# Optimization experiments

Hardware: AMD Instinct MI355X
Metric: run time of the kernel (lower is better)

Reference implementation:

```python
import jax, jax.numpy as jnp
import numpy as np

EPS = 1e-12  # F.normalize default eps


def _wn_weight(v, g):
    # PyTorch weight_norm over dims (in, kernel) per output channel
    norm = jnp.sqrt(jnp.sum(v * v, axis=1, keepdims=True))
    return g[:, None] * v / norm


def _l2_normalize(x, axis=-1):
    n = jnp.sqrt(jnp.sum(x * x, axis=axis, keepdims=True))
    return x / jnp.maximum(n, EPS)


def setup_inputs() -> dict:
    key = jax.random.key(0)
    ks = jax.random.split(key, 8)
    B, D_IN, T = 16, 1024, 2048
    K, D_CB = 4096, 256
    s = 0.02
    return {
        "z": jax.random.normal(ks[0], (B, D_IN, T), dtype=jnp.float32),
        "in_v": jax.random.normal(ks[1], (D_CB, D_IN), dtype=jnp.float32) * s,
        "in_g": jax.random.uniform(ks[2], (D_CB,), dtype=jnp.float32, minval=0.5, maxval=1.5),
        "in_b": jax.random.normal(ks[3], (D_CB,), dtype=jnp.float32) * s,
        "out_v": jax.random.normal(ks[4], (D_IN, D_CB), dtype=jnp.float32) * s,
        "out_g": jax.random.uniform(ks[5], (D_IN,), dtype=jnp.float32, minval=0.5, maxval=1.5),
        "out_b": jax.random.normal(ks[6], (D_IN,), dtype=jnp.float32) * s,
        "codebook": jax.random.normal(ks[7], (K, D_CB), dtype=jnp.float32),
    }


def reference(z, in_v, in_g, in_b, out_v, out_g, out_b, codebook):
    B, _, T = z.shape
    # in_proj: weight-normalized 1x1 conv == per-frame matmul
    W_in = _wn_weight(in_v, in_g)            # (D_cb, D_in)
    z_i = jnp.einsum("oc,bct->bot", W_in, z) + in_b[None, :, None]  # (B, D_cb, T)

    # decode_latents: factorized, L2-normalized nearest-neighbor lookup
    enc = z_i.transpose(0, 2, 1).reshape(-1, z_i.shape[1])  # (B*T, D_cb)
    enc_n = _l2_normalize(enc)
    cb_n = _l2_normalize(codebook)
    dist = (
        jnp.sum(enc_n * enc_n, axis=1, keepdims=True)
        - 2.0 * enc_n @ cb_n.T
        + jnp.sum(cb_n * cb_n, axis=1)[None, :]
    )  # (B*T, K)
    indices = jnp.argmax(-dist, axis=1).reshape(B, T)       # (B, T)
    z_q = codebook[indices].transpose(0, 2, 1)              # (B, D_cb, T)

    # straight-through estimator
    z_q = z_i + jax.lax.stop_gradient(z_q - z_i)

    # out_proj
    W_out = _wn_weight(out_v, out_g)         # (D_in, D_cb)
    z_o = jnp.einsum("oc,bct->bot", W_out, z_q) + out_b[None, :, None]  # (B, D_in, T)
    return (z_i, z_q, z_o, indices)
```

## Files before the change

kernel.cpp:

```cpp
#include <hip/hip_runtime.h>
#include <hip/hip_bf16.h>

#define BATCH 16
#define D_IN  1024
#define T_LEN 2048
#define K_CB  4096
#define D_CB  256

#define ZI_OFF 0
#define ZQ_OFF (BATCH * D_CB * T_LEN)
#define ZO_OFF (ZQ_OFF + BATCH * D_CB * T_LEN)
#define IDX_OFF (ZO_OFF + BATCH * D_IN * T_LEN)

typedef _Float16 half8 __attribute__((ext_vector_type(8)));
typedef _Float16 h4_t  __attribute__((ext_vector_type(4)));
typedef float floatx4 __attribute__((ext_vector_type(4)));

__device__ __forceinline__ float block_sum256(float v) {
    __shared__ float sred[4];
    #pragma unroll
    for (int off = 32; off > 0; off >>= 1) v += __shfl_down(v, off, 64);
    if ((threadIdx.x & 63) == 0) sred[threadIdx.x >> 6] = v;
    __syncthreads();
    float r = sred[0] + sred[1] + sred[2] + sred[3];
    __syncthreads();
    return r;
}

__global__ __launch_bounds__(256) void wn_rows(const float* __restrict__ v,
                                               const float* __restrict__ g,
                                               float* __restrict__ W, int N) {
    int row = blockIdx.x;
    const float* src = v + (size_t)row * N;
    float ss = 0.f;
    for (int c = threadIdx.x; c < N; c += 256) { float x = src[c]; ss += x * x; }
    ss = block_sum256(ss);
    float scale = g[row] * __frsqrt_rn(ss);
    for (int c = threadIdx.x; c < N; c += 256) W[(size_t)row * N + c] = src[c] * scale;
}

__global__ __launch_bounds__(256) void cb_prep(const float* __restrict__ cb,
                                               _Float16* __restrict__ c1,
                                               _Float16* __restrict__ c2) {
    int row = blockIdx.x;
    int c = threadIdx.x;
    float x = cb[(size_t)row * D_CB + c];
    float ss = block_sum256(x * x);
    float scale = 1.0f / fmaxf(sqrtf(ss), 1e-12f);
    float v = x * scale;
    _Float16 h1 = (_Float16)v;
    _Float16 h2 = (_Float16)(v - (float)h1);
    c1[(size_t)row * D_CB + c] = h1;
    c2[(size_t)row * D_CB + c] = h2;
}

template <int KDIM, int M>
__global__ __launch_bounds__(256, 2) void proj_mfma(const float* __restrict__ W,
                                                    const float* __restrict__ bias,
                                                    const float* __restrict__ Z,
                                                    float* __restrict__ Out) {
    __shared__ _Float16 A_s[2][128][40];
    __shared__ _Float16 B_s[2][128][40];

    const int tid  = threadIdx.x;
    const int wv   = tid >> 6;
    const int lane = tid & 63;
    const int lo4  = lane & 15, quad = lane >> 4;
    const int wm   = wv & 1,  wn  = wv >> 1;

    const int f0 = blockIdx.x * 128;
    const int b  = f0 >> 11;
    const int t0 = f0 & (T_LEN - 1);
    const int o0 = blockIdx.y * 128;
    const float* __restrict__ Zb = Z + (size_t)b * KDIM * T_LEN;

    const int a_g  = tid >> 5;
    const int a_tl = tid & 31;

    float  pa[4][4];
    float4 pb[4];

    floatx4 acc[4][4];
    #pragma unroll
    for (int i = 0; i < 4; i++)
        #pragma unroll
        for (int j = 0; j < 4; j++) acc[i][j] = (floatx4){0.f, 0.f, 0.f, 0.f};

    #pragma unroll
    for (int p = 0; p < 4; p++)
        #pragma unroll
        for (int j = 0; j < 4; j++)
            pa[p][j] = Zb[(size_t)(a_g * 4 + j) * T_LEN + t0 + p * 32 + a_tl];
    #pragma unroll
    for (int p = 0; p < 4; p++) {
        int idx = tid + p * 256;
        pb[p] = *(const float4*)&W[(size_t)(o0 + (idx >> 3)) * KDIM + (idx & 7) * 4];
    }

    for (int kk = 0; kk < KDIM; kk += 32) {
        #pragma unroll
        for (int p = 0; p < 4; p++) {
            int f = p * 32 + a_tl;
            h4_t h1, h2;
            #pragma unroll
            for (int j = 0; j < 4; j++) {
                float v = pa[p][j];
                _Float16 x = (_Float16)v;
                h1[j] = x;
                h2[j] = (_Float16)(v - (float)x);
            }
            *(h4_t*)&A_s[0][f][a_g * 4] = h1;
            *(h4_t*)&A_s[1][f][a_g * 4] = h2;
        }
        #pragma unroll
        for (int p = 0; p < 4; p++) {
            int idx = tid + p * 256;
            int o = idx >> 3, k4 = (idx & 7) * 4;
            h4_t h1, h2;
            #pragma unroll
            for (int j = 0; j < 4; j++) {
                float v = ((const float*)&pb[p])[j];
                _Float16 x = (_Float16)v;
                h1[j] = x;
                h2[j] = (_Float16)(v - (float)x);
            }
            *(h4_t*)&B_s[0][o][k4] = h1;
            *(h4_t*)&B_s[1][o][k4] = h2;
        }
        __syncthreads();

        if (kk + 32 < KDIM) {
            #pragma unroll
            for (int p = 0; p < 4; p++)
                #pragma unroll
                for (int j = 0; j < 4; j++)
                    pa[p][j] = Zb[(size_t)(kk + 32 + a_g * 4 + j) * T_LEN + t0 + p * 32 + a_tl];
            #pragma unroll
            for (int p = 0; p < 4; p++) {
                int idx = tid + p * 256;
                pb[p] = *(const float4*)&W[(size_t)(o0 + (idx >> 3)) * KDIM + kk + 32 + (idx & 7) * 4];
            }
        }

        half8 a1[4], a2[4], b1[4], b2[4];
        #pragma unroll
        for (int mi = 0; mi < 4; mi++) {
            a1[mi] = *(const half8*)&A_s[0][wm * 64 + mi * 16 + lo4][quad * 8];
            a2[mi] = *(const half8*)&A_s[1][wm * 64 + mi * 16 + lo4][quad * 8];
        }
        #pragma unroll
        for (int ni = 0; ni < 4; ni++) {
            b1[ni] = *(const half8*)&B_s[0][wn * 64 + ni * 16 + lo4][quad * 8];
            b2[ni] = *(const half8*)&B_s[1][wn * 64 + ni * 16 + lo4][quad * 8];
        }
        #pragma unroll
        for (int mi = 0; mi < 4; mi++)
            #pragma unroll
            for (int ni = 0; ni < 4; ni++) {
                acc[mi][ni] = __builtin_amdgcn_mfma_f32_16x16x32_f16(a1[mi], b1[ni], acc[mi][ni], 0, 0, 0);
                acc[mi][ni] = __builtin_amdgcn_mfma_f32_16x16x32_f16(a1[mi], b2[ni], acc[mi][ni], 0, 0, 0);
                acc[mi][ni] = __builtin_amdgcn_mfma_f32_16x16x32_f16(a2[mi], b1[ni], acc[mi][ni], 0, 0, 0);
            }
        __syncthreads();
    }

    #pragma unroll
    for (int ni = 0; ni < 4; ni++) {
        int o = o0 + wn * 64 + ni * 16 + lo4;
        float bv = bias[o];
        #pragma unroll
        for (int mi = 0; mi < 4; mi++) {
            int t = t0 + wm * 64 + mi * 16 + quad * 4;
            floatx4 r = acc[mi][ni];
            float4 st = make_float4(r[0] + bv, r[1] + bv, r[2] + bv, r[3] + bv);
            *(float4*)&Out[((size_t)b * M + o) * T_LEN + t] = st;
        }
    }
}

__global__ __launch_bounds__(256) void vq_mfma(const float* __restrict__ z_i,
                                               const _Float16* __restrict__ cbn1,
                                               const _Float16* __restrict__ cbn2,
                                               const float* __restrict__ cb,
                                               float* __restrict__ z_q,
                                               float* __restrict__ idx_out) {
    __shared__ _Float16 e_s[2][32][264];
    __shared__ _Float16 cb_s[2][128][72];
    __shared__ float red_v[4][32];
    __shared__ int   red_i[4][32];
    __shared__ int   idx_s[32];

    const int tid  = threadIdx.x;
    const int wv   = tid >> 6;
    const int lane = tid & 63;
    const int lo4  = lane & 15, quad = lane >> 4;
    const int f0 = blockIdx.x * 32;
    const int b  = f0 >> 11;
    const int t0 = f0 & (T_LEN - 1);

    for (int i = tid; i < 32 * 256; i += 256) {
        int k = i >> 5, t = i & 31;
        float v = z_i[((size_t)(b * D_CB + k)) * T_LEN + t0 + t];
        _Float16 h1 = (_Float16)v;
        _Float16 h2 = (_Float16)(v - (float)h1);
        e_s[0][t][k] = h1;
        e_s[1][t][k] = h2;
    }

    float best_v[2][4];
    int   best_i[2][4];
    #pragma unroll
    for (int m = 0; m < 2; m++)
        #pragma unroll
        for (int r = 0; r < 4; r++) { best_v[m][r] = -3.4e38f; best_i[m][r] = 0; }

    __syncthreads();

    for (int n = 0; n < 32; n++) {
        const int cwg = n * 128;
        floatx4 acc[2][2];
        #pragma unroll
        for (int m = 0; m < 2; m++)
            #pragma unroll
            for (int t = 0; t < 2; t++) acc[m][t] = (floatx4){0.f, 0.f, 0.f, 0.f};

        half8 pf[8];
        #pragma unroll
        for (int s = 0; s < 8; s++) {
            int c2 = tid + s * 256;
            const _Float16* src = (s < 4) ? cbn1 : cbn2;
            int rem = c2 & 1023, cw = rem >> 3, ko = (rem & 7) * 8;
            pf[s] = *(const half8*)(src + (size_t)(cwg + cw) * D_CB + ko);
        }

        for (int kc = 0; kc < 4; kc++) {
            #pragma unroll
            for (int s = 0; s < 8; s++) {
                int c2 = tid + s * 256;
                int sp = (s < 4) ? 0 : 1;
                int rem = c2 & 1023, cw = rem >> 3, ko = (rem & 7) * 8;
                *(half8*)&cb_s[sp][cw][ko] = pf[s];
            }
            __syncthreads();
            if (kc < 3) {
                #pragma unroll
                for (int s = 0; s < 8; s++) {
                    int c2 = tid + s * 256;
                    const _Float16* src = (s < 4) ? cbn1 : cbn2;
                    int rem = c2 & 1023, cw = rem >> 3, ko = (rem & 7) * 8;
                    pf[s] = *(const half8*)(src + (size_t)(cwg + cw) * D_CB + (kc + 1) * 64 + ko);
                }
            }
            #pragma unroll
            for (int ks = 0; ks < 2; ks++) {
                const int kb = kc * 64 + ks * 32 + quad * 8;
                const int kl = ks * 32 + quad * 8;
                half8 a1[2], a2[2], b1[2], b2[2];
                #pragma unroll
                for (int m = 0; m < 2; m++) {
                    a1[m] = *(const half8*)&e_s[0][m * 16 + lo4][kb];
                    a2[m] = *(const half8*)&e_s[1][m * 16 + lo4][kb];
                }
                #pragma unroll
                for (int t = 0; t < 2; t++) {
                    b1[t] = *(const half8*)&cb_s[0][wv * 32 + t * 16 + lo4][kl];
                    b2[t] = *(const half8*)&cb_s[1][wv * 32 + t * 16 + lo4][kl];
                }
                #pragma unroll
                for (int m = 0; m < 2; m++)
                    #pragma unroll
                    for (int t = 0; t < 2; t++) {
                        acc[m][t] = __builtin_amdgcn_mfma_f32_16x16x32_f16(a1[m], b1[t], acc[m][t], 0, 0, 0);
                        acc[m][t] = __builtin_amdgcn_mfma_f32_16x16x32_f16(a1[m], b2[t], acc[m][t], 0, 0, 0);
                        acc[m][t] = __builtin_amdgcn_mfma_f32_16x16x32_f16(a2[m], b1[t], acc[m][t], 0, 0, 0);
                    }
            }
            __syncthreads();
        }

        #pragma unroll
        for (int m = 0; m < 2; m++)
            #pragma unroll
            for (int t = 0; t < 2; t++) {
                int cwi = cwg + wv * 32 + t * 16 + lo4;
                #pragma unroll
                for (int r = 0; r < 4; r++) {
                    float v = acc[m][t][r];
                    if (v > best_v[m][r] || (v == best_v[m][r] && cwi < best_i[m][r])) {
                        best_v[m][r] = v; best_i[m][r] = cwi;
                    }
                }
            }
    }

    #pragma unroll
    for (int m = 0; m < 2; m++)
        #pragma unroll
        for (int r = 0; r < 4; r++) {
            float bv = best_v[m][r]; int bi = best_i[m][r];
            #pragma unroll
            for (int off = 8; off > 0; off >>= 1) {
                float ov = __shfl_down(bv, off, 16);
                int   oi = __shfl_down(bi, off, 16);
                if (ov > bv || (ov == bv && oi < bi)) { bv = ov; bi = oi; }
            }
            if (lo4 == 0) {
                red_v[wv][m * 16 + quad * 4 + r] = bv;
                red_i[wv][m * 16 + quad * 4 + r] = bi;
            }
        }
    __syncthreads();
    if (tid < 32) {
        float bv = red_v[0][tid]; int bi = red_i[0][tid];
        #pragma unroll
        for (int w = 1; w < 4; w++) {
            float ov = red_v[w][tid]; int oi = red_i[w][tid];
            if (ov > bv || (ov == bv && oi < bi)) { bv = ov; bi = oi; }
        }
        idx_s[tid] = bi;
        idx_out[f0 + tid] = (float)bi;
    }
    __syncthreads();

    for (int i = tid; i < 32 * 256; i += 256) {
        int k = i >> 5, t = i & 31;
        z_q[((size_t)(b * D_CB + k)) * T_LEN + t0 + t] = cb[(size_t)idx_s[t] * D_CB + k];
    }
}

extern "C" void kernel_launch(void* const* d_in, const int* in_sizes, int n_in,
                              void* d_out, int out_size, void* d_ws, size_t ws_size,
                              hipStream_t stream) {
    const float* z     = (const float*)d_in[0];
    const float* in_v  = (const float*)d_in[1];
    const float* in_g  = (const float*)d_in[2];
    const float* in_b  = (const float*)d_in[3];
    const float* out_v = (const float*)d_in[4];
    const float* out_g = (const float*)d_in[5];
    const float* out_b = (const float*)d_in[6];
    const float* cb    = (const float*)d_in[7];

    float* ws    = (float*)d_ws;
    float* W_in  = ws;
    float* W_out = ws + 262144;
    _Float16* cbn1 = (_Float16*)(ws + 524288);
    _Float16* cbn2 = (_Float16*)(ws + 1048576);

    float* out  = (float*)d_out;
    float* z_i  = out + ZI_OFF;
    float* z_q  = out + ZQ_OFF;
    float* z_o  = out + ZO_OFF;
    float* idxf = out + IDX_OFF;

    wn_rows<<<D_CB, 256, 0, stream>>>(in_v, in_g, W_in, D_IN);
    wn_rows<<<D_IN, 256, 0, stream>>>(out_v, out_g, W_out, D_CB);
    cb_prep<<<K_CB, 256, 0, stream>>>(cb, cbn1, cbn2);

    proj_mfma<D_IN, D_CB><<<dim3((BATCH * T_LEN) / 128, D_CB / 128), 256, 0, stream>>>(W_in, in_b, z, z_i);

    vq_mfma<<<(BATCH * T_LEN) / 32, 256, 0, stream>>>(z_i, cbn1, cbn2, cb, z_q, idxf);

    proj_mfma<D_CB, D_IN><<<dim3((BATCH * T_LEN) / 128, D_IN / 128), 256, 0, stream>>>(W_out, out_b, z_q, z_o);
}
```

Baseline: 691.5 us.

## Pre-swizzle codebook into MFMA fragment layout and stream it directly to registers

The codebook prep kernel now writes the hi/lo fp16 split of the normalized codebook in a tiled layout matching the MFMA B-operand fragment order, interleaving hi and lo parts. The VQ kernel drops the shared-memory codebook staging and its barriers. It keeps the full A fragments (encodings) in registers and has each wave stream its own slice of the codebook from global/L2 with a one-tile register prefetch. Splitting the accumulators into two chains adds MFMA independence, and launch bounds request two blocks per CU. The cost is much higher register pressure and no shared reuse of codebook data across the four waves, so global/L2 traffic goes up.

```diff
diff --git a/kernel.cpp b/kernel.cpp
--- a/kernel.cpp
+++ b/kernel.cpp
@@ -40,8 +40,7 @@
 }
 
 __global__ __launch_bounds__(256) void cb_prep(const float* __restrict__ cb,
-                                               _Float16* __restrict__ c1,
-                                               _Float16* __restrict__ c2) {
+                                               _Float16* __restrict__ cbt) {
     int row = blockIdx.x;
     int c = threadIdx.x;
     float x = cb[(size_t)row * D_CB + c];
@@ -50,8 +49,11 @@
     float v = x * scale;
     _Float16 h1 = (_Float16)v;
     _Float16 h2 = (_Float16)(v - (float)h1);
-    c1[(size_t)row * D_CB + c] = h1;
-    c2[(size_t)row * D_CB + c] = h2;
+    int tt = row >> 4, lo4 = row & 15;
+    int ks = c >> 5, quad = (c >> 3) & 3, j = c & 7;
+    size_t base = ((size_t)(tt * 16 + ks * 2)) * 512 + (quad * 16 + lo4) * 8 + j;
+    cbt[base] = h1;
+    cbt[base + 512] = h2;
 }
 
 template <int KDIM, int M>
@@ -178,14 +180,12 @@
     }
 }
 
-__global__ __launch_bounds__(256) void vq_mfma(const float* __restrict__ z_i,
-                                               const _Float16* __restrict__ cbn1,
-                                               const _Float16* __restrict__ cbn2,
-                                               const float* __restrict__ cb,
-                                               float* __restrict__ z_q,
-                                               float* __restrict__ idx_out) {
+__global__ __launch_bounds__(256, 2) void vq_mfma(const float* __restrict__ z_i,
+                                                  const _Float16* __restrict__ cbt,
+                                                  const float* __restrict__ cb,
+                                                  float* __restrict__ z_q,
+                                                  float* __restrict__ idx_out) {
     __shared__ _Float16 e_s[2][32][264];
-    __shared__ _Float16 cb_s[2][128][72];
     __shared__ float red_v[4][32];
     __shared__ int   red_i[4][32];
     __shared__ int   idx_s[32];
@@ -206,6 +206,16 @@
         e_s[0][t][k] = h1;
         e_s[1][t][k] = h2;
     }
+    __syncthreads();
+
+    half8 a1[2][8], a2[2][8];
+    #pragma unroll
+    for (int m = 0; m < 2; m++)
+        #pragma unroll
+        for (int ks = 0; ks < 8; ks++) {
+            a1[m][ks] = *(const half8*)&e_s[0][m * 16 + lo4][ks * 32 + quad * 8];
+            a2[m][ks] = *(const half8*)&e_s[1][m * 16 + lo4][ks * 32 + quad * 8];
+        }
 
     float best_v[2][4];
     int   best_i[2][4];
@@ -214,81 +224,45 @@
         #pragma unroll
         for (int r = 0; r < 4; r++) { best_v[m][r] = -3.4e38f; best_i[m][r] = 0; }
 
-    __syncthreads();
-
-    for (int n = 0; n < 32; n++) {
-        const int cwg = n * 128;
-        floatx4 acc[2][2];
+    const int tt0 = wv * 64;
+    const _Float16* cb_lane = cbt + lane * 8;
+
+    half8 b1[8], b2[8];
+    #pragma unroll
+    for (int ks = 0; ks < 8; ks++) {
+        b1[ks] = *(const half8*)(cb_lane + (size_t)tt0 * 8192 + ks * 1024);
+        b2[ks] = *(const half8*)(cb_lane + (size_t)tt0 * 8192 + ks * 1024 + 512);
+    }
+
+    for (int tt = tt0; tt < tt0 + 64; tt++) {
+        floatx4 accA[2], accB[2];
+        #pragma unroll
+        for (int m = 0; m < 2; m++) { accA[m] = (floatx4){0.f,0.f,0.f,0.f}; accB[m] = (floatx4){0.f,0.f,0.f,0.f}; }
+
+        const int ttn = (tt + 1 < tt0 + 64) ? tt + 1 : tt0;
+        const _Float16* nb = cb_lane + (size_t)ttn * 8192;
+
+        #pragma unroll
+        for (int ks = 0; ks < 8; ks++) {
+            half8 cb1 = b1[ks], cb2 = b2[ks];
+            accA[0] = __builtin_amdgcn_mfma_f32_16x16x32_f16(a1[0][ks], cb1, accA[0], 0, 0, 0);
+            accB[0] = __builtin_amdgcn_mfma_f32_16x16x32_f16(a1[0][ks], cb2, accB[0], 0, 0, 0);
+            accA[0] = __builtin_amdgcn_mfma_f32_16x16x32_f16(a2[0][ks], cb1, accA[0], 0, 0, 0);
+            accA[1] = __builtin_amdgcn_mfma_f32_16x16x32_f16(a1[1][ks], cb1, accA[1], 0, 0, 0);
+            accB[1] = __builtin_amdgcn_mfma_f32_16x16x32_f16(a1[1][ks], cb2, accB[1], 0, 0, 0);
+            accA[1] = __builtin_amdgcn_mfma_f32_16x16x32_f16(a2[1][ks], cb1, accA[1], 0, 0, 0);
+            b1[ks] = *(const half8*)(nb + ks * 1024);
+            b2[ks] = *(const half8*)(nb + ks * 1024 + 512);
+        }
+
+        const int cwi = tt * 16 + lo4;
         #pragma unroll
         for (int m = 0; m < 2; m++)
             #pragma unroll
-            for (int t = 0; t < 2; t++) acc[m][t] = (floatx4){0.f, 0.f, 0.f, 0.f};
-
-        half8 pf[8];
-        #pragma unroll
-        for (int s = 0; s < 8; s++) {
-            int c2 = tid + s * 256;
-            const _Float16* src = (s < 4) ? cbn1 : cbn2;
-            int rem = c2 & 1023, cw = rem >> 3, ko = (rem & 7) * 8;
-            pf[s] = *(const half8*)(src + (size_t)(cwg + cw) * D_CB + ko);
-        }
-
-        for (int kc = 0; kc < 4; kc++) {
-            #pragma unroll
-            for (int s = 0; s < 8; s++) {
-                int c2 = tid + s * 256;
-                int sp = (s < 4) ? 0 : 1;
-                int rem = c2 & 1023, cw = rem >> 3, ko = (rem & 7) * 8;
-                *(half8*)&cb_s[sp][cw][ko] = pf[s];
-            }
-            __syncthreads();
-            if (kc < 3) {
-                #pragma unroll
-                for (int s = 0; s < 8; s++) {
-                    int c2 = tid + s * 256;
-                    const _Float16* src = (s < 4) ? cbn1 : cbn2;
-                    int rem = c2 & 1023, cw = rem >> 3, ko = (rem & 7) * 8;
-                    pf[s] = *(const half8*)(src + (size_t)(cwg + cw) * D_CB + (kc + 1) * 64 + ko);
-                }
-            }
-            #pragma unroll
-            for (int ks = 0; ks < 2; ks++) {
-                const int kb = kc * 64 + ks * 32 + quad * 8;
-                const int kl = ks * 32 + quad * 8;
-                half8 a1[2], a2[2], b1[2], b2[2];
-                #pragma unroll
-                for (int m = 0; m < 2; m++) {
-                    a1[m] = *(const half8*)&e_s[0][m * 16 + lo4][kb];
-                    a2[m] = *(const half8*)&e_s[1][m * 16 + lo4][kb];
-                }
-                #pragma unroll
-                for (int t = 0; t < 2; t++) {
-                    b1[t] = *(const half8*)&cb_s[0][wv * 32 + t * 16 + lo4][kl];
-                    b2[t] = *(const half8*)&cb_s[1][wv * 32 + t * 16 + lo4][kl];
-                }
-                #pragma unroll
-                for (int m = 0; m < 2; m++)
-                    #pragma unroll
-                    for (int t = 0; t < 2; t++) {
-                        acc[m][t] = __builtin_amdgcn_mfma_f32_16x16x32_f16(a1[m], b1[t], acc[m][t], 0, 0, 0);
-                        acc[m][t] = __builtin_amdgcn_mfma_f32_16x16x32_f16(a1[m], b2[t], acc[m][t], 0, 0, 0);
-                        acc[m][t] = __builtin_amdgcn_mfma_f32_16x16x32_f16(a2[m], b1[t], acc[m][t], 0, 0, 0);
-                    }
-            }
-            __syncthreads();
-        }
-
-        #pragma unroll
-        for (int m = 0; m < 2; m++)
-            #pragma unroll
-            for (int t = 0; t < 2; t++) {
-                int cwi = cwg + wv * 32 + t * 16 + lo4;
-                #pragma unroll
-                for (int r = 0; r < 4; r++) {
-                    float v = acc[m][t][r];
-                    if (v > best_v[m][r] || (v == best_v[m][r] && cwi < best_i[m][r])) {
-                        best_v[m][r] = v; best_i[m][r] = cwi;
-                    }
+            for (int r = 0; r < 4; r++) {
+                float v = accA[m][r] + accB[m][r];
+                if (v > best_v[m][r] || (v == best_v[m][r] && cwi < best_i[m][r])) {
+                    best_v[m][r] = v; best_i[m][r] = cwi;
                 }
             }
     }
@@ -343,8 +317,7 @@
     float* ws    = (float*)d_ws;
     float* W_in  = ws;
     float* W_out = ws + 262144;
-    _Float16* cbn1 = (_Float16*)(ws + 524288);
-    _Float16* cbn2 = (_Float16*)(ws + 1048576);
+    _Float16* cbt = (_Float16*)(ws + 524288);
 
     float* out  = (float*)d_out;
     float* z_i  = out + ZI_OFF;
@@ -354,11 +327,11 @@
 
     wn_rows<<<D_CB, 256, 0, stream>>>(in_v, in_g, W_in, D_IN);
     wn_rows<<<D_IN, 256, 0, stream>>>(out_v, out_g, W_out, D_CB);
-    cb_prep<<<K_CB, 256, 0, stream>>>(cb, cbn1, cbn2);
+    cb_prep<<<K_CB, 256, 0, stream>>>(cb, cbt);
 
     proj_mfma<D_IN, D_CB><<<dim3((BATCH * T_LEN) / 128, D_CB / 128), 256, 0, stream>>>(W_in, in_b, z, z_i);
 
-    vq_mfma<<<(BATCH * T_LEN) / 32, 256, 0, stream>>>(z_i, cbn1, cbn2, cb, z_q, idxf);
+    vq_mfma<<<(BATCH * T_LEN) / 32, 256, 0, stream>>>(z_i, cbt, cb, z_q, idxf);
 
     proj_mfma<D_CB, D_IN><<<dim3((BATCH * T_LEN) / 128, D_IN / 128), 256, 0, stream>>>(W_out, out_b, z_q, z_o);
 }
```

Result: faster. 586.4 us (-15.2%).
